# Performance work log

Hardware: AMD Instinct MI355X
Metric: run time of the kernel (lower is better)

Reference implementation:

```python
import jax, jax.numpy as jnp
import numpy as np
import math

B, H, S, D = 2, 8, 1024, 384
LAMBDA_INIT = 0.8 - 0.6 * math.exp(-0.3 * 1)  # depth = 1


def _clin(xr, xi, wr, wi, br=None, bi=None):
    # complex linear: (xr + i xi) @ (wr + i wi)^T + (br + i bi)
    o_r = jnp.einsum('bhse,de->bhsd', xr, wr) - jnp.einsum('bhse,de->bhsd', xi, wi)
    o_i = jnp.einsum('bhse,de->bhsd', xr, wi) + jnp.einsum('bhse,de->bhsd', xi, wr)
    if br is not None:
        o_r = o_r + br
        o_i = o_i + bi
    return o_r, o_i


def _attn_w(qr, qi, kr, ki, scale):
    # complex score magnitude -> softmax
    s_r = jnp.einsum('bhqd,bhkd->bhqk', qr, kr) + jnp.einsum('bhqd,bhkd->bhqk', qi, ki)
    s_i = jnp.einsum('bhqd,bhkd->bhqk', qi, kr) - jnp.einsum('bhqd,bhkd->bhqk', qr, ki)
    return jax.nn.softmax(jnp.sqrt(s_r ** 2 + s_i ** 2 + 1e-8) * scale, axis=-1)


def setup_inputs() -> dict:
    key = jax.random.key(0)
    ks = jax.random.split(key, 32)
    n = lambda k, sh, std=1.0: jax.random.normal(k, sh, dtype=jnp.float32) * std
    sd = 1.0 / math.sqrt(D)
    inp = {
        'q_r': n(ks[0], (B, H, S, D)), 'q_i': n(ks[1], (B, H, S, D)),
        'k_r': n(ks[2], (B, H, S, D)), 'k_i': n(ks[3], (B, H, S, D)),
        'v_r': n(ks[4], (B, H, S, D)), 'v_i': n(ks[5], (B, H, S, D)),
        'pe_q_r': n(ks[6], (B, H, S, D)), 'pe_q_i': n(ks[7], (B, H, S, D)),
        'pe_k_r': n(ks[8], (B, H, S, D)), 'pe_k_i': n(ks[9], (B, H, S, D)),
        'wq_r': n(ks[10], (2 * D, D), sd), 'wq_i': n(ks[11], (2 * D, D), sd),
        'bq_r': jnp.zeros((2 * D,), jnp.float32), 'bq_i': jnp.zeros((2 * D,), jnp.float32),
        'wk_r': n(ks[12], (D, D), sd), 'wk_i': n(ks[13], (D, D), sd),
        'bk_r': jnp.zeros((D,), jnp.float32), 'bk_i': jnp.zeros((D,), jnp.float32),
        'wv_r': n(ks[14], (D, D), sd), 'wv_i': n(ks[15], (D, D), sd),
        'bv_r': jnp.zeros((D,), jnp.float32), 'bv_i': jnp.zeros((D,), jnp.float32),
        'wg_r': n(ks[16], (D, D), sd), 'wg_i': n(ks[17], (D, D), sd),
        'bg_r': jnp.zeros((D,), jnp.float32), 'bg_i': jnp.zeros((D,), jnp.float32),
        'wo_r': n(ks[18], (D, D), sd), 'wo_i': n(ks[19], (D, D), sd),
        'bo_r': jnp.zeros((D,), jnp.float32), 'bo_i': jnp.zeros((D,), jnp.float32),
        'lam_q1': n(ks[20], (D,), 0.1), 'lam_k1': n(ks[21], (D,), 0.1),
        'lam_q2': n(ks[22], (D,), 0.1), 'lam_k2': n(ks[23], (D,), 0.1),
        'subln_w': jnp.ones((2 * D,), jnp.float32),
    }
    return inp


def reference(q_r, q_i, k_r, k_i, v_r, v_i, pe_q_r, pe_q_i, pe_k_r, pe_k_i,
              wq_r, wq_i, bq_r, bq_i, wk_r, wk_i, bk_r, bk_i,
              wv_r, wv_i, bv_r, bv_i, wg_r, wg_i, bg_r, bg_i,
              wo_r, wo_i, bo_r, bo_i, lam_q1, lam_k1, lam_q2, lam_k2, subln_w):
    scale = D ** (-0.5)
    qp_r, qp_i = _clin(q_r, q_i, wq_r, wq_i, bq_r, bq_i)   # [B,H,S,2D]
    kp_r, kp_i = _clin(k_r, k_i, wk_r, wk_i, bk_r, bk_i)   # [B,H,S,D]
    vp_r, vp_i = _clin(v_r, v_i, wv_r, wv_i, bv_r, bv_i)
    qp_r = qp_r + jnp.concatenate([pe_q_r, pe_q_r], axis=-1)
    qp_i = qp_i + jnp.concatenate([pe_q_i, pe_q_i], axis=-1)
    kp_r = kp_r + pe_k_r
    kp_i = kp_i + pe_k_i
    q1_r, q2_r = jnp.split(qp_r, 2, axis=-1)
    q1_i, q2_i = jnp.split(qp_i, 2, axis=-1)
    w1 = _attn_w(q1_r, q1_i, kp_r, kp_i, scale)
    w2 = _attn_w(q2_r, q2_i, kp_r, kp_i, scale)
    a1_r = jnp.einsum('bhqk,bhkd->bhqd', w1, vp_r)
    a1_i = jnp.einsum('bhqk,bhkd->bhqd', w1, vp_i)
    a2_r = jnp.einsum('bhqk,bhkd->bhqd', w2, vp_r)
    a2_i = jnp.einsum('bhqk,bhkd->bhqd', w2, vp_i)
    cat_r = jnp.concatenate([a1_r, a2_r], axis=-1)
    cat_i = jnp.concatenate([a1_i, a2_i], axis=-1)
    # complex RMSNorm (SubLN) over 2D dim
    rms = jnp.sqrt(jnp.mean(cat_r ** 2 + cat_i ** 2, axis=-1, keepdims=True) + 1e-5)
    cat_r = cat_r / rms * subln_w
    cat_i = cat_i / rms * subln_w
    a1_r, a2_r = jnp.split(cat_r, 2, axis=-1)
    a1_i, a2_i = jnp.split(cat_i, 2, axis=-1)
    lam1 = jnp.exp(jnp.sum(lam_q1 * lam_k1))
    lam2 = jnp.exp(jnp.sum(lam_q2 * lam_k2))
    lam = jax.nn.sigmoid(lam1 - lam2 + LAMBDA_INIT)
    out_r = a1_r - lam * a2_r
    out_i = a1_i - lam * a2_i
    g_r, g_i = _clin(q_r, q_i, wg_r, wg_i, bg_r, bg_i)
    out_r, out_i = g_r * out_r - g_i * out_i, g_r * out_i + g_i * out_r
    out_r, out_i = _clin(out_r, out_i, wo_r, wo_i, bo_r, bo_i)
    return (out_r, out_i)
```

## Files before the change

### kernel.cpp

```cpp
#include <hip/hip_runtime.h>
#include <cstdint>


typedef _Float16 f16;
typedef __attribute__((ext_vector_type(8))) _Float16 f16x8;
typedef __attribute__((ext_vector_type(4))) float    f32x4;

#define NROW      16384L
#define HALF_OUT  6291456L
#define SCALE_QK  0.05103103630798288f
#define LAMBDA_INIT 0.35550906759096926f

__device__ __forceinline__ void gl2lds16(const void* g, void* l) {
  __builtin_amdgcn_global_load_lds(
      (const __attribute__((address_space(1))) void*)(uintptr_t)g,
      (__attribute__((address_space(3))) void*)(uint32_t)(uintptr_t)l,
      16, 0, 0);
}

struct PeTab { const float* p[4]; float sgn[4]; };

enum { MODE_PROJ = 0, MODE_VT = 1, MODE_OUT = 2, MODE_PV = 3 };

template <int MODE>
__launch_bounds__(256, 2)
__global__ void gemm_kernel(const f16* __restrict__ A, int lda, long aBatch,
                            const f16* __restrict__ W, int ldw, long wBatch,
                            const float* __restrict__ bias, PeTab pe,
                            void* __restrict__ outp, int ldo, int K)
{
  __shared__ f16 As[128 * 32];
  __shared__ f16 Bs[128 * 32];
  const int t    = threadIdx.x;
  const int lane = t & 63;
  const int wave = t >> 6;
  const int z    = blockIdx.z;
  const long row0 = (long)blockIdx.y * 128;
  const long col0 = (long)blockIdx.x * 128;
  const f16* Ab = A + z * aBatch + row0 * (long)lda;
  const f16* Wb = W + z * wBatch + col0 * (long)ldw;

  const int wm = (wave >> 1) * 64;
  const int wn = (wave & 1) * 64;
  const int lm = lane & 15;
  const int lk = (lane >> 4) * 8;

  f32x4 acc[4][4] = {};

  for (int kk = 0; kk < K; kk += 32) {
#pragma unroll
    for (int j = 0; j < 2; ++j) {
      int sg = j * 256 + t;
      int r  = sg >> 2;
      int c  = (sg & 3) << 3;
      gl2lds16(Ab + (long)r * lda + (kk + c), &As[sg * 8]);
      gl2lds16(Wb + (long)r * ldw + (kk + c), &Bs[sg * 8]);
    }
    __syncthreads();
    f16x8 bfr[4];
#pragma unroll
    for (int nt = 0; nt < 4; ++nt)
      bfr[nt] = *(const f16x8*)&Bs[(wn + nt * 16 + lm) * 32 + lk];
#pragma unroll
    for (int mt = 0; mt < 4; ++mt) {
      f16x8 afr = *(const f16x8*)&As[(wm + mt * 16 + lm) * 32 + lk];
#pragma unroll
      for (int nt = 0; nt < 4; ++nt)
        acc[mt][nt] = __builtin_amdgcn_mfma_f32_16x16x32_f16(afr, bfr[nt], acc[mt][nt], 0, 0, 0);
    }
    __syncthreads();
  }

  const int lm4 = (lane >> 4) * 4;
  const int ln  = lane & 15;
#pragma unroll
  for (int mt = 0; mt < 4; ++mt) {
#pragma unroll
    for (int nt = 0; nt < 4; ++nt) {
      int col = (int)col0 + wn + nt * 16 + ln;
#pragma unroll
      for (int r = 0; r < 4; ++r) {
        long row = row0 + wm + mt * 16 + lm4 + r;
        float c = acc[mt][nt][r];
        if (MODE == MODE_PROJ) {
          c += bias[col];
          int sct = col >> 8;
          (void)sct;
          int s2 = col / 384;
          int d  = col - s2 * 384;
          const float* pp = pe.p[s2 & 3];
          if (s2 < 4 && pp) c += pe.sgn[s2 & 3] * pp[row * 384 + d];
          ((f16*)outp)[row * (long)ldo + col] = (f16)c;
        } else if (MODE == MODE_VT) {
          c += bias[col];
          long bh = row >> 10, sx = row & 1023;
          ((f16*)outp)[(bh * 768 + col) * 1024 + sx] = (f16)c;
        } else if (MODE == MODE_OUT) {
          c += bias[col];
          float* of = (float*)outp;
          if (col < 384) of[row * 384 + col] = c;
          else           of[HALF_OUT + row * 384 + (col - 384)] = c;
        } else {
          ((f16*)outp)[((long)z * 1024 + row) * 768 + col] = (f16)c;
        }
      }
    }
  }
}

__launch_bounds__(256, 2)
__global__ void score_kernel(const f16* __restrict__ Q2, const f16* __restrict__ Kc,
                             f16* __restrict__ P)
{
  __shared__ f16 AsL[128 * 32], AsH[128 * 32], BsL[128 * 32], BsH[128 * 32];
  const int t = threadIdx.x, lane = t & 63, wave = t >> 6;
  const int z = blockIdx.z, w = z >> 4, bh = z & 15;
  const long row0 = (long)blockIdx.y * 128, col0 = (long)blockIdx.x * 128;
  const f16* A = Q2 + (long)bh * 1024 * 1536 + row0 * 1536 + w * 768;
  const f16* B = Kc + (long)bh * 1024 * 768 + col0 * 768;
  f16* Pz = P + (long)z * 1024 * 1024;

  const int wm = (wave >> 1) * 64, wn = (wave & 1) * 64;
  const int lm = lane & 15, lk = (lane >> 4) * 8;
  f32x4 accr[4][4] = {}, acci[4][4] = {};

  for (int kk = 0; kk < 384; kk += 32) {
#pragma unroll
    for (int j = 0; j < 2; ++j) {
      int sg = j * 256 + t, r = sg >> 2, c = (sg & 3) << 3;
      gl2lds16(A + (long)r * 1536 + kk + c,       &AsL[sg * 8]);
      gl2lds16(A + (long)r * 1536 + 384 + kk + c, &AsH[sg * 8]);
      gl2lds16(B + (long)r * 768 + kk + c,        &BsL[sg * 8]);
      gl2lds16(B + (long)r * 768 + 384 + kk + c,  &BsH[sg * 8]);
    }
    __syncthreads();
    f16x8 bl[4], bh2[4];
#pragma unroll
    for (int nt = 0; nt < 4; ++nt) {
      bl[nt]  = *(const f16x8*)&BsL[(wn + nt * 16 + lm) * 32 + lk];
      bh2[nt] = *(const f16x8*)&BsH[(wn + nt * 16 + lm) * 32 + lk];
    }
#pragma unroll
    for (int mt = 0; mt < 4; ++mt) {
      f16x8 al  = *(const f16x8*)&AsL[(wm + mt * 16 + lm) * 32 + lk];
      f16x8 ah  = *(const f16x8*)&AsH[(wm + mt * 16 + lm) * 32 + lk];
      f16x8 nal = -al;
#pragma unroll
      for (int nt = 0; nt < 4; ++nt) {
        accr[mt][nt] = __builtin_amdgcn_mfma_f32_16x16x32_f16(al,  bl[nt],  accr[mt][nt], 0, 0, 0);
        accr[mt][nt] = __builtin_amdgcn_mfma_f32_16x16x32_f16(ah,  bh2[nt], accr[mt][nt], 0, 0, 0);
        acci[mt][nt] = __builtin_amdgcn_mfma_f32_16x16x32_f16(ah,  bl[nt],  acci[mt][nt], 0, 0, 0);
        acci[mt][nt] = __builtin_amdgcn_mfma_f32_16x16x32_f16(nal, bh2[nt], acci[mt][nt], 0, 0, 0);
      }
    }
    __syncthreads();
  }
  const int lm4 = (lane >> 4) * 4, ln = lane & 15;
#pragma unroll
  for (int mt = 0; mt < 4; ++mt)
#pragma unroll
    for (int nt = 0; nt < 4; ++nt) {
      int col = (int)col0 + wn + nt * 16 + ln;
#pragma unroll
      for (int r = 0; r < 4; ++r) {
        long row = row0 + wm + mt * 16 + lm4 + r;
        float sr = accr[mt][nt][r], si = acci[mt][nt][r];
        float m = sqrtf(sr * sr + si * si + 1e-8f) * SCALE_QK;
        Pz[row * 1024 + col] = (f16)m;
      }
    }
}

__global__ void softmax_kernel(f16* __restrict__ P)
{
  const long row = blockIdx.x;
  f16* p = P + row * 1024;
  const int lane = threadIdx.x;
  f16x8 v0 = *(const f16x8*)(p + lane * 16);
  f16x8 v1 = *(const f16x8*)(p + lane * 16 + 8);
  float x[16];
#pragma unroll
  for (int i = 0; i < 8; ++i) { x[i] = (float)v0[i]; x[8 + i] = (float)v1[i]; }
  float m = x[0];
#pragma unroll
  for (int i = 1; i < 16; ++i) m = fmaxf(m, x[i]);
#pragma unroll
  for (int off = 1; off < 64; off <<= 1) m = fmaxf(m, __shfl_xor(m, off));
  float s = 0.f;
#pragma unroll
  for (int i = 0; i < 16; ++i) { x[i] = __expf(x[i] - m); s += x[i]; }
#pragma unroll
  for (int off = 1; off < 64; off <<= 1) s += __shfl_xor(s, off);
  float inv = 1.f / s;
  f16x8 o0, o1;
#pragma unroll
  for (int i = 0; i < 8; ++i) { o0[i] = (f16)(x[i] * inv); o1[i] = (f16)(x[8 + i] * inv); }
  *(f16x8*)(p + lane * 16)     = o0;
  *(f16x8*)(p + lane * 16 + 8) = o1;
}

__global__ void fuse_kernel(const f16* __restrict__ A1, const f16* __restrict__ A2,
                            const f16* __restrict__ G, const float* __restrict__ subw,
                            const float* __restrict__ lamp, f16* __restrict__ Xatt)
{
  const long row = blockIdx.x;
  const int t = threadIdx.x, lane = t & 63, wv = t >> 6;
  const f16* a1 = A1 + row * 768;
  const f16* a2 = A2 + row * 768;
  const f16* g  = G + row * 768;
  float a1r[3], a1i[3], a2r[3], a2i[3];
  float ss = 0.f;
#pragma unroll
  for (int q = 0; q < 3; ++q) {
    int d = t + q * 128;
    a1r[q] = (float)a1[d]; a1i[q] = (float)a1[d + 384];
    a2r[q] = (float)a2[d]; a2i[q] = (float)a2[d + 384];
    ss += a1r[q] * a1r[q] + a1i[q] * a1i[q] + a2r[q] * a2r[q] + a2i[q] * a2i[q];
  }
#pragma unroll
  for (int m = 1; m < 64; m <<= 1) ss += __shfl_xor(ss, m);
  __shared__ float part[2];
  if (lane == 0) part[wv] = ss;
  __syncthreads();
  float inv = rsqrtf((part[0] + part[1]) * (1.f / 768.f) + 1e-5f);
  float lam = lamp[0];
#pragma unroll
  for (int q = 0; q < 3; ++q) {
    int d = t + q * 128;
    float w1 = subw[d], w2 = subw[d + 384];
    float n1r = a1r[q] * inv * w1, n1i = a1i[q] * inv * w1;
    float n2r = a2r[q] * inv * w2, n2i = a2i[q] * inv * w2;
    float orr = n1r - lam * n2r, oii = n1i - lam * n2i;
    float gr = (float)g[d], gi = (float)g[d + 384];
    Xatt[row * 768 + d]       = (f16)(gr * orr - gi * oii);
    Xatt[row * 768 + d + 384] = (f16)(gr * oii + gi * orr);
  }
}

__global__ void lam_kernel(const float* lq1, const float* lk1,
                           const float* lq2, const float* lk2, float* out)
{
  const int t = threadIdx.x, lane = t & 63, wv = t >> 6;
  float s1 = 0.f, s2 = 0.f;
#pragma unroll
  for (int q = 0; q < 3; ++q) {
    int d = t + q * 128;
    s1 += lq1[d] * lk1[d];
    s2 += lq2[d] * lk2[d];
  }
#pragma unroll
  for (int m = 1; m < 64; m <<= 1) { s1 += __shfl_xor(s1, m); s2 += __shfl_xor(s2, m); }
  __shared__ float p1[2], p2[2];
  if (lane == 0) { p1[wv] = s1; p2[wv] = s2; }
  __syncthreads();
  if (t == 0) {
    float x = expf(p1[0] + p1[1]) - expf(p2[0] + p2[1]) + LAMBDA_INIT;
    out[0] = 1.f / (1.f + expf(-x));
  }
}

__global__ void pack_x(const float* __restrict__ xr, const float* __restrict__ xi,
                       f16* __restrict__ X)
{
  long i = (long)blockIdx.x * 256 + threadIdx.x;
  long row = i / 768;
  int  c   = (int)(i - row * 768);
  float v = (c < 384) ? xr[row * 384 + c] : xi[row * 384 + (c - 384)];
  X[i] = (f16)v;
}

__global__ void pack_wq(const float* wq_r, const float* wq_i,
                        const float* wg_r, const float* wg_i,
                        const float* bq_r, const float* bq_i,
                        const float* bg_r, const float* bg_i,
                        f16* __restrict__ Wp, float* __restrict__ bp)
{
  long i = (long)blockIdx.x * 256 + threadIdx.x;
  int n = (int)(i / 768), e = (int)(i % 768);
  int s = n / 384, d = n - s * 384;
  int hb = (e >= 384);
  int ee = e - hb * 384;
  float v = 0.f, b = 0.f;
  switch (s) {
    case 0: v = hb ? -wq_i[d * 384 + ee]         :  wq_r[d * 384 + ee];         b = bq_r[d];       break;
    case 1: v = hb ?  wq_r[d * 384 + ee]         :  wq_i[d * 384 + ee];         b = bq_i[d];       break;
    case 2: v = hb ? -wq_i[(384 + d) * 384 + ee] :  wq_r[(384 + d) * 384 + ee]; b = bq_r[384 + d]; break;
    case 3: v = hb ?  wq_r[(384 + d) * 384 + ee] :  wq_i[(384 + d) * 384 + ee]; b = bq_i[384 + d]; break;
    case 4: v = hb ? -wg_i[d * 384 + ee]         :  wg_r[d * 384 + ee];         b = bg_r[d];       break;
    case 5: v = hb ?  wg_r[d * 384 + ee]         :  wg_i[d * 384 + ee];         b = bg_i[d];       break;
  }
  Wp[i] = (f16)v;
  if (e == 0) bp[n] = b;
}

__global__ void pack_w_std(const float* wr, const float* wi,
                           const float* br, const float* bi,
                           f16* __restrict__ Wp, float* __restrict__ bp)
{
  long i = (long)blockIdx.x * 256 + threadIdx.x;
  int n = (int)(i / 768), e = (int)(i % 768);
  int hb = (e >= 384);
  int ee = e - hb * 384;
  float v, b;
  if (n < 384) { v = hb ? -wi[n * 384 + ee] : wr[n * 384 + ee]; b = br[n]; }
  else { int d = n - 384; v = hb ? wr[d * 384 + ee] : wi[d * 384 + ee]; b = bi[d]; }
  Wp[i] = (f16)v;
  if (e == 0) bp[n] = b;
}

extern "C" void kernel_launch(void* const* d_in, const int* in_sizes, int n_in,
                              void* d_out, int out_size, void* d_ws, size_t ws_size,
                              hipStream_t stream)
{
  const float* q_r    = (const float*)d_in[0];
  const float* q_i    = (const float*)d_in[1];
  const float* k_r    = (const float*)d_in[2];
  const float* k_i    = (const float*)d_in[3];
  const float* v_r    = (const float*)d_in[4];
  const float* v_i    = (const float*)d_in[5];
  const float* pe_q_r = (const float*)d_in[6];
  const float* pe_q_i = (const float*)d_in[7];
  const float* pe_k_r = (const float*)d_in[8];
  const float* pe_k_i = (const float*)d_in[9];
  const float* wq_r = (const float*)d_in[10];
  const float* wq_i = (const float*)d_in[11];
  const float* bq_r = (const float*)d_in[12];
  const float* bq_i = (const float*)d_in[13];
  const float* wk_r = (const float*)d_in[14];
  const float* wk_i = (const float*)d_in[15];
  const float* bk_r = (const float*)d_in[16];
  const float* bk_i = (const float*)d_in[17];
  const float* wv_r = (const float*)d_in[18];
  const float* wv_i = (const float*)d_in[19];
  const float* bv_r = (const float*)d_in[20];
  const float* bv_i = (const float*)d_in[21];
  const float* wg_r = (const float*)d_in[22];
  const float* wg_i = (const float*)d_in[23];
  const float* bg_r = (const float*)d_in[24];
  const float* bg_i = (const float*)d_in[25];
  const float* wo_r = (const float*)d_in[26];
  const float* wo_i = (const float*)d_in[27];
  const float* bo_r = (const float*)d_in[28];
  const float* bo_i = (const float*)d_in[29];
  const float* lam_q1 = (const float*)d_in[30];
  const float* lam_k1 = (const float*)d_in[31];
  const float* lam_q2 = (const float*)d_in[32];
  const float* lam_k2 = (const float*)d_in[33];
  const float* subln_w = (const float*)d_in[34];

  char* base = (char*)d_ws;
  size_t off = 0;
  auto alloc = [&](size_t bytes) -> void* {
    void* p = base + off;
    off = (off + bytes + 255) & ~(size_t)255;
    return p;
  };
  f16*   Wq   = (f16*)alloc(2304L * 768 * 2);
  f16*   Wk   = (f16*)alloc(768L * 768 * 2);
  f16*   Wv   = (f16*)alloc(768L * 768 * 2);
  f16*   Wo   = (f16*)alloc(768L * 768 * 2);
  float* bq   = (float*)alloc(2304 * 4);
  float* bk   = (float*)alloc(768 * 4);
  float* bv   = (float*)alloc(768 * 4);
  float* bo   = (float*)alloc(768 * 4);
  float* lamp = (float*)alloc(4);
  f16*   X    = (f16*)alloc(NROW * 768 * 2);
  f16*   Q2   = (f16*)alloc(NROW * 1536 * 2);
  f16*   G    = (f16*)alloc(NROW * 768 * 2);
  f16*   Kc   = (f16*)alloc(NROW * 768 * 2);
  f16*   Vt   = (f16*)alloc(16L * 768 * 1024 * 2);
  f16*   P    = (f16*)alloc(32L * 1024 * 1024 * 2);
  if (off > ws_size) return;
  f16* A1   = Q2;
  f16* A2   = Q2 + NROW * 768;
  f16* Xatt = Kc;

  pack_wq<<<6912, 256, 0, stream>>>(wq_r, wq_i, wg_r, wg_i, bq_r, bq_i, bg_r, bg_i, Wq, bq);
  pack_w_std<<<2304, 256, 0, stream>>>(wk_r, wk_i, bk_r, bk_i, Wk, bk);
  pack_w_std<<<2304, 256, 0, stream>>>(wv_r, wv_i, bv_r, bv_i, Wv, bv);
  pack_w_std<<<2304, 256, 0, stream>>>(wo_r, wo_i, bo_r, bo_i, Wo, bo);
  lam_kernel<<<1, 128, 0, stream>>>(lam_q1, lam_k1, lam_q2, lam_k2, lamp);

  PeTab pe0{};

  pack_x<<<49152, 256, 0, stream>>>(q_r, q_i, X);
  PeTab peQ{};
  peQ.p[0] = pe_q_r; peQ.sgn[0] = 1.f;
  peQ.p[1] = pe_q_i; peQ.sgn[1] = 1.f;
  peQ.p[2] = pe_q_r; peQ.sgn[2] = 1.f;
  peQ.p[3] = pe_q_i; peQ.sgn[3] = 1.f;
  gemm_kernel<MODE_PROJ><<<dim3(12, 128, 1), 256, 0, stream>>>(
      X, 768, 0, Wq, 768, 0, bq, peQ, Q2, 1536, 768);
  gemm_kernel<MODE_PROJ><<<dim3(6, 128, 1), 256, 0, stream>>>(
      X, 768, 0, Wq + 1536L * 768, 768, 0, bq + 1536, pe0, G, 768, 768);

  pack_x<<<49152, 256, 0, stream>>>(k_r, k_i, X);
  PeTab peK{};
  peK.p[0] = pe_k_r; peK.sgn[0] = 1.f;
  peK.p[1] = pe_k_i; peK.sgn[1] = 1.f;
  gemm_kernel<MODE_PROJ><<<dim3(6, 128, 1), 256, 0, stream>>>(
      X, 768, 0, Wk, 768, 0, bk, peK, Kc, 768, 768);

  pack_x<<<49152, 256, 0, stream>>>(v_r, v_i, X);
  gemm_kernel<MODE_VT><<<dim3(6, 128, 1), 256, 0, stream>>>(
      X, 768, 0, Wv, 768, 0, bv, pe0, Vt, 0, 768);

  score_kernel<<<dim3(8, 8, 32), 256, 0, stream>>>(Q2, Kc, P);
  softmax_kernel<<<32768, 64, 0, stream>>>(P);
  gemm_kernel<MODE_PV><<<dim3(6, 8, 16), 256, 0, stream>>>(
      P, 1024, 1024L * 1024, Vt, 1024, 768L * 1024, nullptr, pe0, A1, 0, 1024);
  gemm_kernel<MODE_PV><<<dim3(6, 8, 16), 256, 0, stream>>>(
      P + 16L * 1024 * 1024, 1024, 1024L * 1024, Vt, 1024, 768L * 1024, nullptr, pe0, A2, 0, 1024);

  fuse_kernel<<<16384, 128, 0, stream>>>(A1, A2, G, subln_w, lamp, Xatt);

  gemm_kernel<MODE_OUT><<<dim3(6, 128, 1), 256, 0, stream>>>(
      Xatt, 768, 0, Wo, 768, 0, bo, pe0, d_out, 0, 768);

  (void)in_sizes; (void)n_in; (void)out_size;
}
```

Measured before the change: 896.6 us.

## Double-buffer GEMM LDS tiles, merge Q/G projection, fuse both PV products

```diff
diff --git a/kernel.cpp b/kernel.cpp
--- a/kernel.cpp
+++ b/kernel.cpp
@@ -18,54 +18,62 @@
       16, 0, 0);
 }
 
-struct PeTab { const float* p[4]; float sgn[4]; };
-
-enum { MODE_PROJ = 0, MODE_VT = 1, MODE_OUT = 2, MODE_PV = 3 };
-
-template <int MODE>
+struct PeTab { const float* p[6]; float sgn[6]; };
+
+enum { MODE_PROJ = 0, MODE_VT = 1, MODE_OUT = 2 };
+
+template <int MODE, int BN>
 __launch_bounds__(256, 2)
-__global__ void gemm_kernel(const f16* __restrict__ A, int lda, long aBatch,
-                            const f16* __restrict__ W, int ldw, long wBatch,
+__global__ void gemm_kernel(const f16* __restrict__ A, int lda,
+                            const f16* __restrict__ W, int ldw,
                             const float* __restrict__ bias, PeTab pe,
                             void* __restrict__ outp, int ldo, int K)
 {
-  __shared__ f16 As[128 * 32];
-  __shared__ f16 Bs[128 * 32];
+  constexpr int NT = BN / 32;
+  __shared__ f16 As[2][128 * 32];
+  __shared__ f16 Bs[2][BN * 32];
   const int t    = threadIdx.x;
   const int lane = t & 63;
   const int wave = t >> 6;
-  const int z    = blockIdx.z;
   const long row0 = (long)blockIdx.y * 128;
-  const long col0 = (long)blockIdx.x * 128;
-  const f16* Ab = A + z * aBatch + row0 * (long)lda;
-  const f16* Wb = W + z * wBatch + col0 * (long)ldw;
+  const long col0 = (long)blockIdx.x * BN;
+  const f16* Ab = A + row0 * (long)lda;
+  const f16* Wb = W + col0 * (long)ldw;
 
   const int wm = (wave >> 1) * 64;
-  const int wn = (wave & 1) * 64;
+  const int wn = (wave & 1) * (BN / 2);
   const int lm = lane & 15;
   const int lk = (lane >> 4) * 8;
 
-  f32x4 acc[4][4] = {};
-
-  for (int kk = 0; kk < K; kk += 32) {
+  f32x4 acc[4][NT] = {};
+
+  auto stage = [&](int kk, int buf) {
 #pragma unroll
     for (int j = 0; j < 2; ++j) {
-      int sg = j * 256 + t;
-      int r  = sg >> 2;
-      int c  = (sg & 3) << 3;
-      gl2lds16(Ab + (long)r * lda + (kk + c), &As[sg * 8]);
-      gl2lds16(Wb + (long)r * ldw + (kk + c), &Bs[sg * 8]);
-    }
-    __syncthreads();
-    f16x8 bfr[4];
-#pragma unroll
-    for (int nt = 0; nt < 4; ++nt)
-      bfr[nt] = *(const f16x8*)&Bs[(wn + nt * 16 + lm) * 32 + lk];
+      int sg = j * 256 + t, r = sg >> 2, c = (sg & 3) << 3;
+      gl2lds16(Ab + (long)r * lda + kk + c, &As[buf][sg * 8]);
+    }
+#pragma unroll
+    for (int j = 0; j < BN / 64; ++j) {
+      int sg = j * 256 + t, r = sg >> 2, c = (sg & 3) << 3;
+      gl2lds16(Wb + (long)r * ldw + kk + c, &Bs[buf][sg * 8]);
+    }
+  };
+
+  stage(0, 0);
+  __syncthreads();
+  int buf = 0;
+  for (int kk = 0; kk < K; kk += 32, buf ^= 1) {
+    if (kk + 32 < K) stage(kk + 32, buf ^ 1);
+    f16x8 bfr[NT];
+#pragma unroll
+    for (int nt = 0; nt < NT; ++nt)
+      bfr[nt] = *(const f16x8*)&Bs[buf][(wn + nt * 16 + lm) * 32 + lk];
 #pragma unroll
     for (int mt = 0; mt < 4; ++mt) {
-      f16x8 afr = *(const f16x8*)&As[(wm + mt * 16 + lm) * 32 + lk];
-#pragma unroll
-      for (int nt = 0; nt < 4; ++nt)
+      f16x8 afr = *(const f16x8*)&As[buf][(wm + mt * 16 + lm) * 32 + lk];
+#pragma unroll
+      for (int nt = 0; nt < NT; ++nt)
         acc[mt][nt] = __builtin_amdgcn_mfma_f32_16x16x32_f16(afr, bfr[nt], acc[mt][nt], 0, 0, 0);
     }
     __syncthreads();
@@ -76,7 +84,7 @@
 #pragma unroll
   for (int mt = 0; mt < 4; ++mt) {
 #pragma unroll
-    for (int nt = 0; nt < 4; ++nt) {
+    for (int nt = 0; nt < NT; ++nt) {
       int col = (int)col0 + wn + nt * 16 + ln;
 #pragma unroll
       for (int r = 0; r < 4; ++r) {
@@ -84,24 +92,20 @@
         float c = acc[mt][nt][r];
         if (MODE == MODE_PROJ) {
           c += bias[col];
-          int sct = col >> 8;
-          (void)sct;
           int s2 = col / 384;
           int d  = col - s2 * 384;
-          const float* pp = pe.p[s2 & 3];
-          if (s2 < 4 && pp) c += pe.sgn[s2 & 3] * pp[row * 384 + d];
+          const float* pp = pe.p[s2];
+          if (pp) c += pe.sgn[s2] * pp[row * 384 + d];
           ((f16*)outp)[row * (long)ldo + col] = (f16)c;
         } else if (MODE == MODE_VT) {
           c += bias[col];
           long bh = row >> 10, sx = row & 1023;
           ((f16*)outp)[(bh * 768 + col) * 1024 + sx] = (f16)c;
-        } else if (MODE == MODE_OUT) {
+        } else {
           c += bias[col];
           float* of = (float*)outp;
           if (col < 384) of[row * 384 + col] = c;
           else           of[HALF_OUT + row * 384 + (col - 384)] = c;
-        } else {
-          ((f16*)outp)[((long)z * 1024 + row) * 768 + col] = (f16)c;
         }
       }
     }
@@ -109,14 +113,15 @@
 }
 
 __launch_bounds__(256, 2)
-__global__ void score_kernel(const f16* __restrict__ Q2, const f16* __restrict__ Kc,
+__global__ void score_kernel(const f16* __restrict__ QG, const f16* __restrict__ Kc,
                              f16* __restrict__ P)
 {
-  __shared__ f16 AsL[128 * 32], AsH[128 * 32], BsL[128 * 32], BsH[128 * 32];
+  __shared__ f16 AsL[2][128 * 32], AsH[2][128 * 32];
+  __shared__ f16 BsL[2][128 * 32], BsH[2][128 * 32];
   const int t = threadIdx.x, lane = t & 63, wave = t >> 6;
   const int z = blockIdx.z, w = z >> 4, bh = z & 15;
   const long row0 = (long)blockIdx.y * 128, col0 = (long)blockIdx.x * 128;
-  const f16* A = Q2 + (long)bh * 1024 * 1536 + row0 * 1536 + w * 768;
+  const f16* A = QG + (long)bh * 1024 * 2304 + row0 * 2304 + w * 768;
   const f16* B = Kc + (long)bh * 1024 * 768 + col0 * 768;
   f16* Pz = P + (long)z * 1024 * 1024;
 
@@ -124,26 +129,32 @@
   const int lm = lane & 15, lk = (lane >> 4) * 8;
   f32x4 accr[4][4] = {}, acci[4][4] = {};
 
-  for (int kk = 0; kk < 384; kk += 32) {
+  auto stage = [&](int kk, int buf) {
 #pragma unroll
     for (int j = 0; j < 2; ++j) {
       int sg = j * 256 + t, r = sg >> 2, c = (sg & 3) << 3;
-      gl2lds16(A + (long)r * 1536 + kk + c,       &AsL[sg * 8]);
-      gl2lds16(A + (long)r * 1536 + 384 + kk + c, &AsH[sg * 8]);
-      gl2lds16(B + (long)r * 768 + kk + c,        &BsL[sg * 8]);
-      gl2lds16(B + (long)r * 768 + 384 + kk + c,  &BsH[sg * 8]);
-    }
-    __syncthreads();
+      gl2lds16(A + (long)r * 2304 + kk + c,       &AsL[buf][sg * 8]);
+      gl2lds16(A + (long)r * 2304 + 384 + kk + c, &AsH[buf][sg * 8]);
+      gl2lds16(B + (long)r * 768 + kk + c,        &BsL[buf][sg * 8]);
+      gl2lds16(B + (long)r * 768 + 384 + kk + c,  &BsH[buf][sg * 8]);
+    }
+  };
+
+  stage(0, 0);
+  __syncthreads();
+  int buf = 0;
+  for (int kk = 0; kk < 384; kk += 32, buf ^= 1) {
+    if (kk + 32 < 384) stage(kk + 32, buf ^ 1);
     f16x8 bl[4], bh2[4];
 #pragma unroll
     for (int nt = 0; nt < 4; ++nt) {
-      bl[nt]  = *(const f16x8*)&BsL[(wn + nt * 16 + lm) * 32 + lk];
-      bh2[nt] = *(const f16x8*)&BsH[(wn + nt * 16 + lm) * 32 + lk];
+      bl[nt]  = *(const f16x8*)&BsL[buf][(wn + nt * 16 + lm) * 32 + lk];
+      bh2[nt] = *(const f16x8*)&BsH[buf][(wn + nt * 16 + lm) * 32 + lk];
     }
 #pragma unroll
     for (int mt = 0; mt < 4; ++mt) {
-      f16x8 al  = *(const f16x8*)&AsL[(wm + mt * 16 + lm) * 32 + lk];
-      f16x8 ah  = *(const f16x8*)&AsH[(wm + mt * 16 + lm) * 32 + lk];
+      f16x8 al  = *(const f16x8*)&AsL[buf][(wm + mt * 16 + lm) * 32 + lk];
+      f16x8 ah  = *(const f16x8*)&AsH[buf][(wm + mt * 16 + lm) * 32 + lk];
       f16x8 nal = -al;
 #pragma unroll
       for (int nt = 0; nt < 4; ++nt) {
@@ -171,6 +182,68 @@
     }
 }
 
+__launch_bounds__(256, 2)
+__global__ void pv_kernel(const f16* __restrict__ P, const f16* __restrict__ Vt,
+                          f16* __restrict__ O1, f16* __restrict__ O2)
+{
+  __shared__ f16 As1[2][128 * 32], As2[2][128 * 32], Bs[2][128 * 32];
+  const int t = threadIdx.x, lane = t & 63, wave = t >> 6;
+  const int bh = blockIdx.z;
+  const long row0 = (long)blockIdx.y * 128, col0 = (long)blockIdx.x * 128;
+  const f16* A1 = P + ((long)bh << 20) + row0 * 1024;
+  const f16* A2 = P + ((long)(16 + bh) << 20) + row0 * 1024;
+  const f16* B  = Vt + (long)bh * 768 * 1024 + col0 * 1024;
+
+  const int wm = (wave >> 1) * 64, wn = (wave & 1) * 64;
+  const int lm = lane & 15, lk = (lane >> 4) * 8;
+  f32x4 ac1[4][4] = {}, ac2[4][4] = {};
+
+  auto stage = [&](int kk, int buf) {
+#pragma unroll
+    for (int j = 0; j < 2; ++j) {
+      int sg = j * 256 + t, r = sg >> 2, c = (sg & 3) << 3;
+      gl2lds16(A1 + (long)r * 1024 + kk + c, &As1[buf][sg * 8]);
+      gl2lds16(A2 + (long)r * 1024 + kk + c, &As2[buf][sg * 8]);
+      gl2lds16(B  + (long)r * 1024 + kk + c, &Bs[buf][sg * 8]);
+    }
+  };
+
+  stage(0, 0);
+  __syncthreads();
+  int buf = 0;
+  for (int kk = 0; kk < 1024; kk += 32, buf ^= 1) {
+    if (kk + 32 < 1024) stage(kk + 32, buf ^ 1);
+    f16x8 bfr[4];
+#pragma unroll
+    for (int nt = 0; nt < 4; ++nt)
+      bfr[nt] = *(const f16x8*)&Bs[buf][(wn + nt * 16 + lm) * 32 + lk];
+#pragma unroll
+    for (int mt = 0; mt < 4; ++mt) {
+      f16x8 a1 = *(const f16x8*)&As1[buf][(wm + mt * 16 + lm) * 32 + lk];
+      f16x8 a2 = *(const f16x8*)&As2[buf][(wm + mt * 16 + lm) * 32 + lk];
+#pragma unroll
+      for (int nt = 0; nt < 4; ++nt) {
+        ac1[mt][nt] = __builtin_amdgcn_mfma_f32_16x16x32_f16(a1, bfr[nt], ac1[mt][nt], 0, 0, 0);
+        ac2[mt][nt] = __builtin_amdgcn_mfma_f32_16x16x32_f16(a2, bfr[nt], ac2[mt][nt], 0, 0, 0);
+      }
+    }
+    __syncthreads();
+  }
+  const int lm4 = (lane >> 4) * 4, ln = lane & 15;
+#pragma unroll
+  for (int mt = 0; mt < 4; ++mt)
+#pragma unroll
+    for (int nt = 0; nt < 4; ++nt) {
+      int col = (int)col0 + wn + nt * 16 + ln;
+#pragma unroll
+      for (int r = 0; r < 4; ++r) {
+        long row = (long)bh * 1024 + row0 + wm + mt * 16 + lm4 + r;
+        O1[row * 768 + col] = (f16)ac1[mt][nt][r];
+        O2[row * 768 + col] = (f16)ac2[mt][nt][r];
+      }
+    }
+}
+
 __global__ void softmax_kernel(f16* __restrict__ P)
 {
   const long row = blockIdx.x;
@@ -200,14 +273,14 @@
 }
 
 __global__ void fuse_kernel(const f16* __restrict__ A1, const f16* __restrict__ A2,
-                            const f16* __restrict__ G, const float* __restrict__ subw,
+                            const f16* __restrict__ QG, const float* __restrict__ subw,
                             const float* __restrict__ lamp, f16* __restrict__ Xatt)
 {
   const long row = blockIdx.x;
   const int t = threadIdx.x, lane = t & 63, wv = t >> 6;
   const f16* a1 = A1 + row * 768;
   const f16* a2 = A2 + row * 768;
-  const f16* g  = G + row * 768;
+  const f16* g  = QG + row * 2304 + 1536;
   float a1r[3], a1i[3], a2r[3], a2i[3];
   float ss = 0.f;
 #pragma unroll
@@ -365,15 +438,14 @@
   float* bo   = (float*)alloc(768 * 4);
   float* lamp = (float*)alloc(4);
   f16*   X    = (f16*)alloc(NROW * 768 * 2);
-  f16*   Q2   = (f16*)alloc(NROW * 1536 * 2);
-  f16*   G    = (f16*)alloc(NROW * 768 * 2);
+  f16*   QG   = (f16*)alloc(NROW * 2304 * 2);
   f16*   Kc   = (f16*)alloc(NROW * 768 * 2);
   f16*   Vt   = (f16*)alloc(16L * 768 * 1024 * 2);
   f16*   P    = (f16*)alloc(32L * 1024 * 1024 * 2);
   if (off > ws_size) return;
-  f16* A1   = Q2;
-  f16* A2   = Q2 + NROW * 768;
-  f16* Xatt = Kc;
+  f16* A1   = Kc;
+  f16* A2   = X;
+  f16* Xatt = Vt;
 
   pack_wq<<<6912, 256, 0, stream>>>(wq_r, wq_i, wg_r, wg_i, bq_r, bq_i, bg_r, bg_i, Wq, bq);
   pack_w_std<<<2304, 256, 0, stream>>>(wk_r, wk_i, bk_r, bk_i, Wk, bk);
@@ -389,33 +461,28 @@
   peQ.p[1] = pe_q_i; peQ.sgn[1] = 1.f;
   peQ.p[2] = pe_q_r; peQ.sgn[2] = 1.f;
   peQ.p[3] = pe_q_i; peQ.sgn[3] = 1.f;
-  gemm_kernel<MODE_PROJ><<<dim3(12, 128, 1), 256, 0, stream>>>(
-      X, 768, 0, Wq, 768, 0, bq, peQ, Q2, 1536, 768);
-  gemm_kernel<MODE_PROJ><<<dim3(6, 128, 1), 256, 0, stream>>>(
-      X, 768, 0, Wq + 1536L * 768, 768, 0, bq + 1536, pe0, G, 768, 768);
+  gemm_kernel<MODE_PROJ, 256><<<dim3(9, 128), 256, 0, stream>>>(
+      X, 768, Wq, 768, bq, peQ, QG, 2304, 768);
 
   pack_x<<<49152, 256, 0, stream>>>(k_r, k_i, X);
   PeTab peK{};
   peK.p[0] = pe_k_r; peK.sgn[0] = 1.f;
   peK.p[1] = pe_k_i; peK.sgn[1] = 1.f;
-  gemm_kernel<MODE_PROJ><<<dim3(6, 128, 1), 256, 0, stream>>>(
-      X, 768, 0, Wk, 768, 0, bk, peK, Kc, 768, 768);
+  gemm_kernel<MODE_PROJ, 128><<<dim3(6, 128), 256, 0, stream>>>(
+      X, 768, Wk, 768, bk, peK, Kc, 768, 768);
 
   pack_x<<<49152, 256, 0, stream>>>(v_r, v_i, X);
-  gemm_kernel<MODE_VT><<<dim3(6, 128, 1), 256, 0, stream>>>(
-      X, 768, 0, Wv, 768, 0, bv, pe0, Vt, 0, 768);
-
-  score_kernel<<<dim3(8, 8, 32), 256, 0, stream>>>(Q2, Kc, P);
+  gemm_kernel<MODE_VT, 128><<<dim3(6, 128), 256, 0, stream>>>(
+      X, 768, Wv, 768, bv, pe0, Vt, 0, 768);
+
+  score_kernel<<<dim3(8, 8, 32), 256, 0, stream>>>(QG, Kc, P);
   softmax_kernel<<<32768, 64, 0, stream>>>(P);
-  gemm_kernel<MODE_PV><<<dim3(6, 8, 16), 256, 0, stream>>>(
-      P, 1024, 1024L * 1024, Vt, 1024, 768L * 1024, nullptr, pe0, A1, 0, 1024);
-  gemm_kernel<MODE_PV><<<dim3(6, 8, 16), 256, 0, stream>>>(
-      P + 16L * 1024 * 1024, 1024, 1024L * 1024, Vt, 1024, 768L * 1024, nullptr, pe0, A2, 0, 1024);
-
-  fuse_kernel<<<16384, 128, 0, stream>>>(A1, A2, G, subln_w, lamp, Xatt);
-
-  gemm_kernel<MODE_OUT><<<dim3(6, 128, 1), 256, 0, stream>>>(
-      Xatt, 768, 0, Wo, 768, 0, bo, pe0, d_out, 0, 768);
+  pv_kernel<<<dim3(6, 8, 16), 256, 0, stream>>>(P, Vt, A1, A2);
+
+  fuse_kernel<<<16384, 128, 0, stream>>>(A1, A2, QG, subln_w, lamp, Xatt);
+
+  gemm_kernel<MODE_OUT, 128><<<dim3(6, 128), 256, 0, stream>>>(
+      Xatt, 768, Wo, 768, bo, pe0, d_out, 0, 768);
 
   (void)in_sizes; (void)n_in; (void)out_size;
 }
```

Measured after the change: 900.3 us. Within noise of the previous version (+0.4%).
